# Optimization experiments

Measured on AMD Instinct MI355X. Metric: run time of the kernel, lower is better.

Reference implementation:

```python
import jax, jax.numpy as jnp
import numpy as np

BETA, ALPHA, NS_STEPS = 0.9, 1.0, 1
D_MODEL, D_STATE, D_CONV, EXPAND = 768, 16, 4, 2
D_INNER = EXPAND * D_MODEL
DT_RANK = -(-D_MODEL // 16)  # ceil(d_model/16) = 48
B, L = 2, 1024


def setup_inputs() -> dict:
    key = jax.random.key(0)
    ks = jax.random.split(key, 8)
    s = lambda k, shape, sc=0.02: jax.random.normal(k, shape, jnp.float32) * sc
    return {
        "hidden_states": jax.random.normal(ks[0], (B, L, D_MODEL), jnp.float32),
        "in_proj_w": s(ks[1], (2 * D_INNER, D_MODEL)),
        "conv_w": s(ks[2], (D_INNER, 1, D_CONV), 0.2),
        "conv_b": jnp.zeros((D_INNER,), jnp.float32),
        "x_proj_w": s(ks[3], (DT_RANK + 2 * D_STATE, D_INNER)),
        "dt_head_w": s(ks[4], (D_INNER, DT_RANK)),
        "dt_head_b": s(ks[5], (D_INNER,), 0.1),
        "out_proj_w": s(ks[6], (D_MODEL, D_INNER)),
        "D": jnp.ones((D_INNER,), jnp.float32),
    }


def _newton_schulz(G, steps):
    """Muon-style quintic Newton-Schulz orthogonalization of (b, d, n) with d >= n."""
    a, b, c = 3.4445, -4.7750, 2.0315
    X = G / (jnp.linalg.norm(G, axis=(-2, -1), keepdims=True) + 1e-7)
    X = X.swapaxes(-2, -1)  # (b, n, d): rows <= cols
    for _ in range(steps):
        A = X @ X.swapaxes(-2, -1)       # (b, n, n) small Gram
        Bm = b * A + c * (A @ A)
        X = a * X + Bm @ X
    return X.swapaxes(-2, -1)            # back to (b, d, n)


def reference(hidden_states, in_proj_w, conv_w, conv_b, x_proj_w, dt_head_w, dt_head_b, out_proj_w, D):
    Bz, Lz, _ = hidden_states.shape
    dtype = hidden_states.dtype
    # input projection -> x, z  (B, L, d_inner) each
    xz = jnp.einsum('bld,ed->ble', hidden_states, in_proj_w)
    x, z = jnp.split(xz, 2, axis=-1)
    # causal depthwise conv over time + SiLU
    xc = jax.lax.conv_general_dilated(
        x.swapaxes(1, 2), conv_w, (1,), [(D_CONV - 1, 0)],
        dimension_numbers=('NCH', 'OIH', 'NCH'), feature_group_count=D_INNER)
    x = jax.nn.silu(xc.swapaxes(1, 2) + conv_b)  # (B, L, d_inner)
    # projections for dt / k / q
    x_dbl = jnp.einsum('bld,ed->ble', x, x_proj_w)
    dt_low, k, q = jnp.split(x_dbl, [DT_RANK, DT_RANK + D_STATE], axis=-1)
    dt = jnp.einsum('blr,dr->bld', dt_low, dt_head_w)  # (B, L, d_inner), bias applied in scan

    def step(carry, inp):
        v, h = carry  # velocity / hidden states, each (b, d_inner, d_state)
        x_t, dt_t, k_t, q_t = inp
        dt_t = jax.nn.sigmoid(dt_t + dt_head_b)                              # (b, d)
        dt_t = dt_t / (1.0 + dt_t * jnp.sum(k_t * k_t, axis=-1, keepdims=True))
        dA = 1.0 - dt_t[:, :, None] * (k_t * k_t)[:, None, :]                # (b, d, n)
        G = (dt_t * x_t)[:, :, None] * k_t[:, None, :]                       # dt * u * k
        v = BETA * v + ALPHA * _newton_schulz(G, NS_STEPS)
        h = dA * h + v
        y_t = jnp.einsum('bdn,bn->bd', h, q_t) + D * x_t
        return (v, h), y_t

    init = (jnp.zeros((Bz, D_INNER, D_STATE), dtype),
            jnp.zeros((Bz, D_INNER, D_STATE), dtype))
    xs = (x.swapaxes(0, 1), dt.swapaxes(0, 1), k.swapaxes(0, 1), q.swapaxes(0, 1))
    _, y = jax.lax.scan(step, init, xs)        # (L, B, d_inner)
    y = y.swapaxes(0, 1) * jax.nn.silu(z)      # gate
    return jnp.einsum('bld,od->blo', y, out_proj_w)
```

## Files before the change

### kernel.cpp

```cpp
#include <hip/hip_runtime.h>

#define D_MODEL 768
#define D_STATE 16
#define D_INNER 1536
#define DT_RANK 48
#define NB 2
#define LSEQ 1024
#define NROWS (NB * LSEQ)
#define CCH 16
#define CLEN (LSEQ / CCH)
#define STP 16
#define BETA_CL 1.1790185e-03f
#define OUT_ELEMS (NROWS * D_MODEL)

typedef __attribute__((ext_vector_type(4))) float f32x4;
typedef __attribute__((ext_vector_type(8))) short s16x8;
typedef __attribute__((ext_vector_type(8))) unsigned short u16x8;
typedef __attribute__((ext_vector_type(4))) unsigned short u16x4;

__device__ __forceinline__ unsigned short f2bu(float f) {
  unsigned int x = __builtin_bit_cast(unsigned int, f);
  x += 0x7fffu + ((x >> 16) & 1u);
  return (unsigned short)(x >> 16);
}

typedef __attribute__((address_space(3))) unsigned int as3u32;
typedef __attribute__((address_space(1))) const unsigned int as1u32;
__device__ __forceinline__ void gload16(const unsigned short* g, unsigned short* l) {
  __builtin_amdgcn_global_load_lds((as1u32*)g, (as3u32*)l, 16, 0, 0);
}

#define CVT_TOTAL 663552
#define Z1_GROUPS 20480
__global__ __launch_bounds__(256) void cvt5z_kernel(const float* __restrict__ s0,
                                                    const float* __restrict__ s1,
                                                    const float* __restrict__ s2,
                                                    const float* __restrict__ s3,
                                                    const float* __restrict__ s4,
                                                    unsigned short* __restrict__ d0,
                                                    unsigned short* __restrict__ d1,
                                                    unsigned short* __restrict__ d2,
                                                    unsigned short* __restrict__ d3,
                                                    unsigned short* __restrict__ d4,
                                                    float* __restrict__ z1) {
  int g = blockIdx.x * 256 + threadIdx.x;
  if (g >= CVT_TOTAL) {
    int zg = g - CVT_TOTAL;
    f32x4 zero = {0.f, 0.f, 0.f, 0.f};
    if (zg < Z1_GROUPS) {
      *(f32x4*)(z1 + zg * 8) = zero;
      *(f32x4*)(z1 + zg * 8 + 4) = zero;
    }
    return;
  }
  const float* s;
  unsigned short* d;
  int base;
  if (g < 196608)      { s = s0; d = d0; base = 0; }
  else if (g < 491520) { s = s1; d = d1; base = 196608; }
  else if (g < 506880) { s = s2; d = d2; base = 491520; }
  else if (g < 516096) { s = s3; d = d3; base = 506880; }
  else                 { s = s4; d = d4; base = 516096; }
  int i = (g - base) * 8;
  f32x4 a = *(const f32x4*)(s + i);
  f32x4 b = *(const f32x4*)(s + i + 4);
  u16x8 o;
#pragma unroll
  for (int j = 0; j < 4; j++) { o[j] = f2bu(a[j]); o[4 + j] = f2bu(b[j]); }
  *(u16x8*)(d + i) = o;
}

template <bool PARTIAL>
__global__ __launch_bounds__(256) void gemm128(const unsigned short* __restrict__ A,
                                               const unsigned short* __restrict__ B,
                                               float* __restrict__ C, int K,
                                               int lda, int ldb, int ldc, int kseg_len) {
  __shared__ __align__(16) unsigned short As[2][128 * 32];
  __shared__ __align__(16) unsigned short Bs[2][128 * 32];
  const int m0 = blockIdx.y * 128, n0 = blockIdx.x * 128;
  const int kbeg = blockIdx.z * kseg_len;
  const int kend = kbeg + kseg_len;
  const int t = threadIdx.x;
  const int wave = t >> 6, lane = t & 63;
  const int wm = wave >> 1, wn = wave & 1;
  const int quad = lane >> 4, l16 = lane & 15;
  const int srow = lane >> 2;
  const int kcol = (lane & 3) * 8;

  float* Cp = C;
  if constexpr (PARTIAL) Cp = C + (size_t)blockIdx.z * (size_t)gridDim.y * 128 * ldc;

  auto stage = [&](int bi, int k0) {
#pragma unroll
    for (int r = 0; r < 2; r++) {
      const int seg = r * 64 + wave * 16;
      gload16(A + (size_t)(m0 + seg + srow) * lda + k0 + kcol, &As[bi][seg * 32]);
      gload16(B + (size_t)(n0 + seg + srow) * ldb + k0 + kcol, &Bs[bi][seg * 32]);
    }
  };

  f32x4 acc[4][4] = {};
  stage(0, kbeg);
  __syncthreads();
  int buf = 0;
  for (int k0 = kbeg; k0 < kend; k0 += 32) {
    if (k0 + 32 < kend) stage(buf ^ 1, k0 + 32);
    s16x8 af[4], bf[4];
#pragma unroll
    for (int i = 0; i < 4; i++) {
      af[i] = *(const s16x8*)&As[buf][(wm * 64 + i * 16 + l16) * 32 + quad * 8];
      bf[i] = *(const s16x8*)&Bs[buf][(wn * 64 + i * 16 + l16) * 32 + quad * 8];
    }
#pragma unroll
    for (int mi = 0; mi < 4; mi++)
#pragma unroll
      for (int ni = 0; ni < 4; ni++)
        acc[mi][ni] = __builtin_amdgcn_mfma_f32_16x16x32_bf16(af[mi], bf[ni], acc[mi][ni], 0, 0, 0);
    __syncthreads();
    buf ^= 1;
  }
#pragma unroll
  for (int mi = 0; mi < 4; mi++)
#pragma unroll
    for (int ni = 0; ni < 4; ni++)
#pragma unroll
      for (int r = 0; r < 4; r++) {
        int row = m0 + wm * 64 + mi * 16 + quad * 4 + r;
        int col = n0 + wn * 64 + ni * 16 + l16;
        Cp[(size_t)row * ldc + col] = acc[mi][ni][r];
      }
}

__global__ __launch_bounds__(256) void reduce4_kernel(const float* __restrict__ part,
                                                      float* __restrict__ out) {
  int i4 = (blockIdx.x * 256 + threadIdx.x) * 4;
  f32x4 a = *(const f32x4*)(part + i4);
  f32x4 b = *(const f32x4*)(part + (size_t)OUT_ELEMS + i4);
  f32x4 c = *(const f32x4*)(part + (size_t)2 * OUT_ELEMS + i4);
  f32x4 d = *(const f32x4*)(part + (size_t)3 * OUT_ELEMS + i4);
  f32x4 o;
#pragma unroll
  for (int j = 0; j < 4; j++) o[j] = (a[j] + b[j]) + (c[j] + d[j]);
  *(f32x4*)(out + i4) = o;
}

template <bool AF32, bool ATOMIC>
__global__ __launch_bounds__(256) void gemm_bt(const void* __restrict__ Av,
                                               const unsigned short* __restrict__ B,
                                               float* __restrict__ C, int M, int N, int K,
                                               int lda, int ldb, int ldc, int kseg_len) {
  __shared__ __align__(16) unsigned short As[2][64][40];
  __shared__ __align__(16) unsigned short Bs[2][64][40];
  const int m0 = blockIdx.y * 64, n0 = blockIdx.x * 64;
  const int kbeg = blockIdx.z * kseg_len;
  const int kend = (kbeg + kseg_len < K) ? (kbeg + kseg_len) : K;
  const int t = threadIdx.x;
  const int wave = t >> 6, lane = t & 63;
  const int wm = wave >> 1, wn = wave & 1;
  const int quad = lane >> 4, l16 = lane & 15;
  const int srow = t >> 2;
  const int kseg = (t & 3) * 8;
  const bool va = (m0 + srow) < M, vb = (n0 + srow) < N;
  const float* Af = (const float*)Av;
  const unsigned short* Ab = (const unsigned short*)Av;
  const unsigned short* Bp = B + (size_t)(n0 + srow) * ldb;

  f32x4 ra0, ra1;
  u16x8 rab, rbb;
  auto pref = [&](int k0) {
    const int kk = k0 + kseg;
    const int krem = kend - kk;
    if constexpr (AF32) {
      const float* Ap = Af + (size_t)(m0 + srow) * lda + kk;
      if (va && krem >= 8) {
        ra0 = *(const f32x4*)Ap;
        ra1 = *(const f32x4*)(Ap + 4);
      } else {
#pragma unroll
        for (int j = 0; j < 4; j++) {
          ra0[j] = (va && j < krem) ? Ap[j] : 0.0f;
          ra1[j] = (va && j + 4 < krem) ? Ap[j + 4] : 0.0f;
        }
      }
    } else {
      const unsigned short* Ap = Ab + (size_t)(m0 + srow) * lda + kk;
      if (va && krem >= 8) {
        rab = *(const u16x8*)Ap;
      } else {
#pragma unroll
        for (int j = 0; j < 8; j++) rab[j] = (va && j < krem) ? Ap[j] : (unsigned short)0;
      }
    }
    if (vb && krem >= 8) {
      rbb = *(const u16x8*)(Bp + kk);
    } else {
#pragma unroll
      for (int j = 0; j < 8; j++) rbb[j] = (vb && j < krem) ? Bp[kk + j] : (unsigned short)0;
    }
  };
  auto tolds = [&](int bi) {
    if constexpr (AF32) {
      u16x8 oa;
#pragma unroll
      for (int j = 0; j < 4; j++) { oa[j] = f2bu(ra0[j]); oa[4 + j] = f2bu(ra1[j]); }
      *(u16x8*)&As[bi][srow][kseg] = oa;
    } else {
      *(u16x8*)&As[bi][srow][kseg] = rab;
    }
    *(u16x8*)&Bs[bi][srow][kseg] = rbb;
  };

  f32x4 acc[2][2] = {};
  pref(kbeg);
  tolds(0);
  __syncthreads();
  int buf = 0;
  for (int k0 = kbeg; k0 < kend; k0 += 32) {
    const bool more = (k0 + 32 < kend);
    if (more) pref(k0 + 32);
    s16x8 a0 = *(const s16x8*)&As[buf][wm * 32 + l16][quad * 8];
    s16x8 a1 = *(const s16x8*)&As[buf][wm * 32 + 16 + l16][quad * 8];
    s16x8 b0 = *(const s16x8*)&Bs[buf][wn * 32 + l16][quad * 8];
    s16x8 b1 = *(const s16x8*)&Bs[buf][wn * 32 + 16 + l16][quad * 8];
    acc[0][0] = __builtin_amdgcn_mfma_f32_16x16x32_bf16(a0, b0, acc[0][0], 0, 0, 0);
    acc[0][1] = __builtin_amdgcn_mfma_f32_16x16x32_bf16(a0, b1, acc[0][1], 0, 0, 0);
    acc[1][0] = __builtin_amdgcn_mfma_f32_16x16x32_bf16(a1, b0, acc[1][0], 0, 0, 0);
    acc[1][1] = __builtin_amdgcn_mfma_f32_16x16x32_bf16(a1, b1, acc[1][1], 0, 0, 0);
    if (more) tolds(buf ^ 1);
    __syncthreads();
    buf ^= 1;
  }
#pragma unroll
  for (int mi = 0; mi < 2; mi++)
#pragma unroll
    for (int ni = 0; ni < 2; ni++)
#pragma unroll
      for (int r = 0; r < 4; r++) {
        int row = m0 + wm * 32 + mi * 16 + quad * 4 + r;
        int col = n0 + wn * 32 + ni * 16 + l16;
        if (row < M && col < N) {
          if constexpr (ATOMIC)
            atomicAdd(&C[(size_t)row * ldc + col], acc[mi][ni][r]);
          else
            C[(size_t)row * ldc + col] = acc[mi][ni][r];
        }
      }
}

__global__ __launch_bounds__(256) void conv_silu_kernel(const float* __restrict__ xz,
                                                        const float* __restrict__ cw,
                                                        const float* __restrict__ cb,
                                                        float* __restrict__ xc,
                                                        unsigned short* __restrict__ xcb) {
  int g = blockIdx.x * 256 + threadIdx.x;
  int c4 = (g % 384) * 4;
  int row = g / 384;
  int l = row & (LSEQ - 1);
  f32x4 acc = *(const f32x4*)(cb + c4);
  f32x4 w[4];
#pragma unroll
  for (int ci = 0; ci < 4; ci++) w[ci] = *(const f32x4*)(cw + (c4 + ci) * 4);
#pragma unroll
  for (int j = 0; j < 4; j++) {
    int dl = l - 3 + j;
    if (dl >= 0) {
      f32x4 xv = *(const f32x4*)(xz + (size_t)(row - 3 + j) * 3072 + c4);
#pragma unroll
      for (int ci = 0; ci < 4; ci++) acc[ci] = fmaf(xv[ci], w[ci][j], acc[ci]);
    }
  }
  f32x4 val;
  u16x4 ob;
#pragma unroll
  for (int ci = 0; ci < 4; ci++) {
    float sg = 1.0f / (1.0f + expf(-acc[ci]));
    val[ci] = acc[ci] * sg;
    ob[ci] = f2bu(val[ci]);
  }
  *(f32x4*)(xc + (size_t)row * D_INNER + c4) = val;
  *(u16x4*)(xcb + (size_t)row * D_INNER + c4) = ob;
}

__global__ __launch_bounds__(256) void precompute_kernel(const float* __restrict__ xdbl,
                                                         float* __restrict__ dtbuf,
                                                         const float* __restrict__ xconv,
                                                         const float* __restrict__ dtb,
                                                         float* __restrict__ ubuf,
                                                         float* __restrict__ kqbuf) {
  int row = blockIdx.x;
  int t = threadIdx.x;
  const float* xr = xdbl + (size_t)row * 80;
  float nk = 0.0f;
#pragma unroll
  for (int n = 0; n < 16; n++) { float kv = xr[48 + n]; nk += kv * kv; }
  f32x4 dtf[2], u0[2];
  float nupart = 0.0f;
#pragma unroll
  for (int gi = 0; gi < 2; gi++) {
    int g = gi * 256 + t;
    if (g < 384) {
      int d = g * 4;
      f32x4 draw = *(const f32x4*)(dtbuf + (size_t)row * D_INNER + d);
      f32x4 bb = *(const f32x4*)(dtb + d);
      f32x4 xcv = *(const f32x4*)(xconv + (size_t)row * D_INNER + d);
      f32x4 df, uu;
#pragma unroll
      for (int j = 0; j < 4; j++) {
        float sg = 1.0f / (1.0f + expf(-(draw[j] + bb[j])));
        float dv = sg / (1.0f + sg * nk);
        df[j] = dv;
        float u = dv * xcv[j];
        uu[j] = u;
        nupart += u * u;
      }
      dtf[gi] = df;
      u0[gi] = uu;
    }
  }
  __shared__ float red[4];
  float v = nupart;
#pragma unroll
  for (int off = 32; off > 0; off >>= 1) v += __shfl_xor(v, off);
  if ((t & 63) == 0) red[t >> 6] = v;
  __syncthreads();
  float nu = red[0] + red[1] + red[2] + red[3];
  float p = nu * nk;
  float s = sqrtf(p) + 1e-7f;
  float tt = p / (s * s);
  float gamma = (3.4445f + tt * (-4.7750f + 2.0315f * tt)) / s;
#pragma unroll
  for (int gi = 0; gi < 2; gi++) {
    int g = gi * 256 + t;
    if (g < 384) {
      int d = g * 4;
      f32x4 df = dtf[gi], uu = u0[gi], us;
#pragma unroll
      for (int j = 0; j < 4; j++) us[j] = gamma * uu[j];
      *(f32x4*)(dtbuf + (size_t)row * D_INNER + d) = df;
      *(f32x4*)(ubuf + (size_t)row * D_INNER + d) = us;
    }
  }
  if (t < 8)
    *(f32x4*)(kqbuf + (size_t)row * 32 + t * 4) = *(const f32x4*)(xr + 48 + t * 4);
}

__global__ __launch_bounds__(256) void scan_phase1(const float* __restrict__ ubuf,
                                                   const float* __restrict__ dtbuf,
                                                   const float* __restrict__ kqbuf,
                                                   float* __restrict__ cvp,
                                                   float* __restrict__ chp,
                                                   float* __restrict__ gp,
                                                   float* __restrict__ rp) {
  __shared__ __align__(16) float u_s[2][STP][64];
  __shared__ __align__(16) float dt_s[2][STP][64];
  __shared__ __align__(16) float kq_s[2][STP][36];
  const int t = threadIdx.x;
  const int nq = t & 3, dloc = t >> 2;
  const int b = blockIdx.x / (24 * CCH);
  const int rem = blockIdx.x % (24 * CCH);
  const int d0 = (rem / CCH) * 64;
  const int c = rem % CCH;
  const int tbase = c * CLEN;
  const size_t ub = (size_t)b * LSEQ * D_INNER + d0;
  const float* kqb = kqbuf + (size_t)b * LSEQ * 32;
  const int prow = t >> 4, pcol = (t & 15) * 4;
  const int krow = t >> 3, kcol = (t & 7) * 4;
  f32x4 pu, pd, pk;
  auto prefetch = [&](int t0) {
    size_t off = ub + (size_t)(t0 + prow) * D_INNER + pcol;
    pu = *(const f32x4*)(ubuf + off);
    pd = *(const f32x4*)(dtbuf + off);
    if (t < 128) pk = *(const f32x4*)(kqb + (size_t)(t0 + krow) * 32 + kcol);
  };
  auto writelds = [&](int bi) {
    *(f32x4*)&u_s[bi][prow][pcol] = pu;
    *(f32x4*)&dt_s[bi][prow][pcol] = pd;
    if (t < 128) *(f32x4*)&kq_s[bi][krow][kcol] = pk;
  };
  f32x4 v = {0.f, 0.f, 0.f, 0.f}, h = {0.f, 0.f, 0.f, 0.f};
  f32x4 g = {0.f, 0.f, 0.f, 0.f}, r = {1.f, 1.f, 1.f, 1.f};
  float bt = 0.9f;
  prefetch(tbase);
  writelds(0);
  __syncthreads();
  int buf = 0;
  for (int t0 = 0; t0 < CLEN; t0 += STP) {
    const bool more = (t0 + STP < CLEN);
    if (more) prefetch(tbase + t0 + STP);
#pragma unroll 4
    for (int s = 0; s < STP; s++) {
      float u = u_s[buf][s][dloc];
      float dtf = dt_s[buf][s][dloc];
      f32x4 kv = *(const f32x4*)&kq_s[buf][s][nq * 4];
#pragma unroll
      for (int j = 0; j < 4; j++) {
        float kj = kv[j];
        v[j] = fmaf(0.9f, v[j], u * kj);
        float a = fmaf(-dtf * kj, kj, 1.0f);
        h[j] = fmaf(a, h[j], v[j]);
        r[j] *= a;
        g[j] = fmaf(a, g[j], bt);
      }
      bt *= 0.9f;
    }
    if (more) writelds(buf ^ 1);
    __syncthreads();
    buf ^= 1;
  }
  size_t o = (((size_t)b * CCH + c) * D_INNER + d0 + dloc) * 16 + nq * 4;
  *(f32x4*)(cvp + o) = v;
  *(f32x4*)(chp + o) = h;
  *(f32x4*)(gp + o) = g;
  *(f32x4*)(rp + o) = r;
}

__global__ __launch_bounds__(256) void scan_phase2(const float* __restrict__ cvp,
                                                   const float* __restrict__ chp,
                                                   float* __restrict__ gp,
                                                   float* __restrict__ rp) {
  int i4 = (blockIdx.x * 256 + threadIdx.x) * 4;
  int b = i4 / (D_INNER * 16);
  int rem = i4 % (D_INNER * 16);
  f32x4 v0 = {0.f, 0.f, 0.f, 0.f}, h0 = {0.f, 0.f, 0.f, 0.f};
#pragma unroll
  for (int c = 0; c < CCH; c++) {
    size_t o = ((size_t)(b * CCH + c)) * (D_INNER * 16) + rem;
    f32x4 cv = *(const f32x4*)(cvp + o);
    f32x4 ch = *(const f32x4*)(chp + o);
    f32x4 gg = *(const f32x4*)(gp + o);
    f32x4 rr = *(const f32x4*)(rp + o);
    *(f32x4*)(gp + o) = v0;
    *(f32x4*)(rp + o) = h0;
#pragma unroll
    for (int j = 0; j < 4; j++) {
      float v0n = fmaf(BETA_CL, v0[j], cv[j]);
      float h0n = fmaf(gg[j], v0[j], fmaf(rr[j], h0[j], ch[j]));
      v0[j] = v0n;
      h0[j] = h0n;
    }
  }
}

__global__ __launch_bounds__(256) void scan_phase3(const float* __restrict__ ubuf,
                                                   const float* __restrict__ dtbuf,
                                                   const float* __restrict__ kqbuf,
                                                   const float* __restrict__ gp,
                                                   const float* __restrict__ rp,
                                                   const float* __restrict__ xconv,
                                                   const float* __restrict__ xz,
                                                   const float* __restrict__ Dp,
                                                   unsigned short* __restrict__ ygb) {
  __shared__ __align__(16) float u_s[2][STP][64];
  __shared__ __align__(16) float dt_s[2][STP][64];
  __shared__ __align__(16) float xc_s[2][STP][64];
  __shared__ __align__(16) float z_s[2][STP][64];
  __shared__ __align__(16) float kq_s[2][STP][36];
  const int t = threadIdx.x;
  const int nq = t & 3, dloc = t >> 2;
  const int b = blockIdx.x / (24 * CCH);
  const int rem = blockIdx.x % (24 * CCH);
  const int d0 = (rem / CCH) * 64;
  const int c = rem % CCH;
  const int tbase = c * CLEN;
  const size_t ub = (size_t)b * LSEQ * D_INNER + d0;
  const float* kqb = kqbuf + (size_t)b * LSEQ * 32;
  const float* xzb = xz + (size_t)b * LSEQ * 3072 + 1536 + d0;
  unsigned short* y_p = ygb + (size_t)b * LSEQ * D_INNER + d0 + dloc;
  const int prow = t >> 4, pcol = (t & 15) * 4;
  const int krow = t >> 3, kcol = (t & 7) * 4;
  f32x4 pu, pd, pxc, pz, pk;
  auto prefetch = [&](int t0) {
    size_t off = ub + (size_t)(t0 + prow) * D_INNER + pcol;
    pu = *(const f32x4*)(ubuf + off);
    pd = *(const f32x4*)(dtbuf + off);
    pxc = *(const f32x4*)(xconv + off);
    pz = *(const f32x4*)(xzb + (size_t)(t0 + prow) * 3072 + pcol);
    if (t < 128) pk = *(const f32x4*)(kqb + (size_t)(t0 + krow) * 32 + kcol);
  };
  auto writelds = [&](int bi) {
    *(f32x4*)&u_s[bi][prow][pcol] = pu;
    *(f32x4*)&dt_s[bi][prow][pcol] = pd;
    *(f32x4*)&xc_s[bi][prow][pcol] = pxc;
    *(f32x4*)&z_s[bi][prow][pcol] = pz;
    if (t < 128) *(f32x4*)&kq_s[bi][krow][kcol] = pk;
  };
  size_t so = (((size_t)b * CCH + c) * D_INNER + d0 + dloc) * 16 + nq * 4;
  f32x4 v = *(const f32x4*)(gp + so);
  f32x4 h = *(const f32x4*)(rp + so);
  const float Dd = Dp[d0 + dloc];
  prefetch(tbase);
  writelds(0);
  __syncthreads();
  int buf = 0;
  for (int t0 = 0; t0 < CLEN; t0 += STP) {
    const bool more = (t0 + STP < CLEN);
    if (more) prefetch(tbase + t0 + STP);
#pragma unroll 4
    for (int s = 0; s < STP; s++) {
      float u = u_s[buf][s][dloc];
      float dtf = dt_s[buf][s][dloc];
      f32x4 kv = *(const f32x4*)&kq_s[buf][s][nq * 4];
      f32x4 qv = *(const f32x4*)&kq_s[buf][s][16 + nq * 4];
      float yp = 0.0f;
#pragma unroll
      for (int j = 0; j < 4; j++) {
        float kj = kv[j];
        v[j] = fmaf(0.9f, v[j], u * kj);
        float dA = fmaf(-dtf * kj, kj, 1.0f);
        h[j] = fmaf(dA, h[j], v[j]);
        yp = fmaf(h[j], qv[j], yp);
      }
      yp += __shfl_xor(yp, 1);
      yp += __shfl_xor(yp, 2);
      float zv = z_s[buf][s][dloc];
      float sz = zv / (1.0f + expf(-zv));
      float val = (yp + Dd * xc_s[buf][s][dloc]) * sz;
      if (nq == 0) y_p[(size_t)(tbase + t0 + s) * D_INNER] = f2bu(val);
    }
    if (more) writelds(buf ^ 1);
    __syncthreads();
    buf ^= 1;
  }
}

extern "C" void kernel_launch(void* const* d_in, const int* in_sizes, int n_in,
                              void* d_out, int out_size, void* d_ws, size_t ws_size,
                              hipStream_t stream) {
  const float* hidden = (const float*)d_in[0];
  const float* w_in   = (const float*)d_in[1];
  const float* conv_w = (const float*)d_in[2];
  const float* conv_b = (const float*)d_in[3];
  const float* w_x    = (const float*)d_in[4];
  const float* w_dt   = (const float*)d_in[5];
  const float* b_dt   = (const float*)d_in[6];
  const float* w_out  = (const float*)d_in[7];
  const float* Dp     = (const float*)d_in[8];

  float* ws    = (float*)d_ws;
  float* xz    = ws;
  float* xconv = xz + (size_t)NROWS * 3072;
  float* xdbl  = xconv + (size_t)NROWS * D_INNER;
  float* dtbuf = xdbl + (size_t)NROWS * 80;
  float* ubuf  = dtbuf + (size_t)NROWS * D_INNER;
  float* kqbuf = ubuf + (size_t)NROWS * D_INNER;
  const size_t PL = (size_t)NB * CCH * D_INNER * 16;
  float* cvp   = kqbuf + (size_t)NROWS * 32;
  float* chp   = cvp + PL;
  float* gp    = chp + PL;
  float* rp    = gp + PL;
  float* opart = rp + PL;
  unsigned short* bfr = (unsigned short*)(opart + (size_t)4 * OUT_ELEMS);
  unsigned short* hbf = bfr;
  unsigned short* wib = hbf + 1572864;
  unsigned short* wxb = wib + 2359296;
  unsigned short* wdb = wxb + 122880;
  unsigned short* wob = wdb + 73728;
  unsigned short* xcb = wob + 1179648;
  unsigned short* ygb = xcb + 3145728;

  dim3 blk(256);
  cvt5z_kernel<<<dim3((CVT_TOTAL + Z1_GROUPS) / 256), blk, 0, stream>>>(
      hidden, w_in, w_x, w_dt, w_out, hbf, wib, wxb, wdb, wob, xdbl);
  gemm128<false><<<dim3(24, 16, 1), blk, 0, stream>>>(hbf, wib, xz, 768, 768, 768, 3072, 768);
  conv_silu_kernel<<<dim3(3072), blk, 0, stream>>>(xz, conv_w, conv_b, xconv, xcb);
  gemm_bt<false, true><<<dim3(2, 32, 8), blk, 0, stream>>>(xcb, wxb, xdbl, 2048, 80, 1536,
                                                           1536, 1536, 80, 192);
  gemm_bt<true, false><<<dim3(24, 32, 1), blk, 0, stream>>>(xdbl, wdb, dtbuf, 2048, 1536, 48,
                                                            80, 48, 1536, 48);
  precompute_kernel<<<dim3(NROWS), blk, 0, stream>>>(xdbl, dtbuf, xconv, b_dt, ubuf, kqbuf);
  scan_phase1<<<dim3(NB * 24 * CCH), blk, 0, stream>>>(ubuf, dtbuf, kqbuf, cvp, chp, gp, rp);
  scan_phase2<<<dim3(48), blk, 0, stream>>>(cvp, chp, gp, rp);
  scan_phase3<<<dim3(NB * 24 * CCH), blk, 0, stream>>>(ubuf, dtbuf, kqbuf, gp, rp,
                                                       xconv, xz, Dp, ygb);
  gemm128<true><<<dim3(6, 16, 4), blk, 0, stream>>>(ygb, wob, opart, 1536,
                                                    1536, 1536, 768, 384);
  reduce4_kernel<<<dim3(OUT_ELEMS / 1024), blk, 0, stream>>>(opart, (float*)d_out);
}
```

Baseline: 203.4 us.

## Split-K the input projection and recompute scaled u inside the scan

The input-projection GEMM becomes a two-way split-K into two partial buffers. The conv and the phase-3 z loads now sum the two partials on the fly instead of a separate reduce. The precompute kernel no longer writes a full gamma-scaled u tensor; it stores one gamma per row. Both scan phases rebuild u as gamma*dt*xconv from data they already stage in shared memory. This removes one full-size intermediate write and read and adds parallelism to the GEMM, at the cost of doubling the reads of the xz partials.

```diff
diff --git a/kernel.cpp b/kernel.cpp
--- a/kernel.cpp
+++ b/kernel.cpp
@@ -247,7 +247,7 @@
       }
 }
 
-__global__ __launch_bounds__(256) void conv_silu_kernel(const float* __restrict__ xz,
+__global__ __launch_bounds__(256) void conv_silu_kernel(const float* __restrict__ xzp,
                                                         const float* __restrict__ cw,
                                                         const float* __restrict__ cb,
                                                         float* __restrict__ xc,
@@ -256,6 +256,8 @@
   int c4 = (g % 384) * 4;
   int row = g / 384;
   int l = row & (LSEQ - 1);
+  const float* x0 = xzp;
+  const float* x1 = xzp + (size_t)NROWS * 3072;
   f32x4 acc = *(const f32x4*)(cb + c4);
   f32x4 w[4];
 #pragma unroll
@@ -264,9 +266,11 @@
   for (int j = 0; j < 4; j++) {
     int dl = l - 3 + j;
     if (dl >= 0) {
-      f32x4 xv = *(const f32x4*)(xz + (size_t)(row - 3 + j) * 3072 + c4);
-#pragma unroll
-      for (int ci = 0; ci < 4; ci++) acc[ci] = fmaf(xv[ci], w[ci][j], acc[ci]);
+      size_t off = (size_t)(row - 3 + j) * 3072 + c4;
+      f32x4 a0 = *(const f32x4*)(x0 + off);
+      f32x4 a1 = *(const f32x4*)(x1 + off);
+#pragma unroll
+      for (int ci = 0; ci < 4; ci++) acc[ci] = fmaf(a0[ci] + a1[ci], w[ci][j], acc[ci]);
     }
   }
   f32x4 val;
@@ -285,7 +289,7 @@
                                                          float* __restrict__ dtbuf,
                                                          const float* __restrict__ xconv,
                                                          const float* __restrict__ dtb,
-                                                         float* __restrict__ ubuf,
+                                                         float* __restrict__ gammabuf,
                                                          float* __restrict__ kqbuf) {
   int row = blockIdx.x;
   int t = threadIdx.x;
@@ -293,7 +297,6 @@
   float nk = 0.0f;
 #pragma unroll
   for (int n = 0; n < 16; n++) { float kv = xr[48 + n]; nk += kv * kv; }
-  f32x4 dtf[2], u0[2];
   float nupart = 0.0f;
 #pragma unroll
   for (int gi = 0; gi < 2; gi++) {
@@ -303,18 +306,16 @@
       f32x4 draw = *(const f32x4*)(dtbuf + (size_t)row * D_INNER + d);
       f32x4 bb = *(const f32x4*)(dtb + d);
       f32x4 xcv = *(const f32x4*)(xconv + (size_t)row * D_INNER + d);
-      f32x4 df, uu;
+      f32x4 df;
 #pragma unroll
       for (int j = 0; j < 4; j++) {
         float sg = 1.0f / (1.0f + expf(-(draw[j] + bb[j])));
         float dv = sg / (1.0f + sg * nk);
         df[j] = dv;
         float u = dv * xcv[j];
-        uu[j] = u;
         nupart += u * u;
       }
-      dtf[gi] = df;
-      u0[gi] = uu;
+      *(f32x4*)(dtbuf + (size_t)row * D_INNER + d) = df;
     }
   }
   __shared__ float red[4];
@@ -328,32 +329,23 @@
   float s = sqrtf(p) + 1e-7f;
   float tt = p / (s * s);
   float gamma = (3.4445f + tt * (-4.7750f + 2.0315f * tt)) / s;
-#pragma unroll
-  for (int gi = 0; gi < 2; gi++) {
-    int g = gi * 256 + t;
-    if (g < 384) {
-      int d = g * 4;
-      f32x4 df = dtf[gi], uu = u0[gi], us;
-#pragma unroll
-      for (int j = 0; j < 4; j++) us[j] = gamma * uu[j];
-      *(f32x4*)(dtbuf + (size_t)row * D_INNER + d) = df;
-      *(f32x4*)(ubuf + (size_t)row * D_INNER + d) = us;
-    }
-  }
+  if (t == 0) gammabuf[row] = gamma;
   if (t < 8)
     *(f32x4*)(kqbuf + (size_t)row * 32 + t * 4) = *(const f32x4*)(xr + 48 + t * 4);
 }
 
-__global__ __launch_bounds__(256) void scan_phase1(const float* __restrict__ ubuf,
+__global__ __launch_bounds__(256) void scan_phase1(const float* __restrict__ xconv,
                                                    const float* __restrict__ dtbuf,
                                                    const float* __restrict__ kqbuf,
+                                                   const float* __restrict__ gammabuf,
                                                    float* __restrict__ cvp,
                                                    float* __restrict__ chp,
                                                    float* __restrict__ gp,
                                                    float* __restrict__ rp) {
-  __shared__ __align__(16) float u_s[2][STP][64];
+  __shared__ __align__(16) float xc_s[2][STP][64];
   __shared__ __align__(16) float dt_s[2][STP][64];
   __shared__ __align__(16) float kq_s[2][STP][36];
+  __shared__ float g_s[2][STP];
   const int t = threadIdx.x;
   const int nq = t & 3, dloc = t >> 2;
   const int b = blockIdx.x / (24 * CCH);
@@ -361,40 +353,43 @@
   const int d0 = (rem / CCH) * 64;
   const int c = rem % CCH;
   const int tbase = c * CLEN;
-  const size_t ub = (size_t)b * LSEQ * D_INNER + d0;
-  const float* kqb = kqbuf + (size_t)b * LSEQ * 32;
+  const size_t ub = ((size_t)b * LSEQ + tbase) * D_INNER + d0;
+  const float* kqb = kqbuf + ((size_t)b * LSEQ + tbase) * 32;
+  const float* gmb = gammabuf + (size_t)b * LSEQ + tbase;
   const int prow = t >> 4, pcol = (t & 15) * 4;
   const int krow = t >> 3, kcol = (t & 7) * 4;
-  f32x4 pu, pd, pk;
+  f32x4 pxc, pd, pk;
+  float pg;
   auto prefetch = [&](int t0) {
     size_t off = ub + (size_t)(t0 + prow) * D_INNER + pcol;
-    pu = *(const f32x4*)(ubuf + off);
+    pxc = *(const f32x4*)(xconv + off);
     pd = *(const f32x4*)(dtbuf + off);
     if (t < 128) pk = *(const f32x4*)(kqb + (size_t)(t0 + krow) * 32 + kcol);
+    if (t < STP) pg = gmb[t0 + t];
   };
   auto writelds = [&](int bi) {
-    *(f32x4*)&u_s[bi][prow][pcol] = pu;
+    *(f32x4*)&xc_s[bi][prow][pcol] = pxc;
     *(f32x4*)&dt_s[bi][prow][pcol] = pd;
     if (t < 128) *(f32x4*)&kq_s[bi][krow][kcol] = pk;
+    if (t < STP) g_s[bi][t] = pg;
   };
   f32x4 v = {0.f, 0.f, 0.f, 0.f}, h = {0.f, 0.f, 0.f, 0.f};
   f32x4 g = {0.f, 0.f, 0.f, 0.f}, r = {1.f, 1.f, 1.f, 1.f};
   float bt = 0.9f;
-  prefetch(tbase);
+  prefetch(0);
   writelds(0);
   __syncthreads();
   int buf = 0;
   for (int t0 = 0; t0 < CLEN; t0 += STP) {
     const bool more = (t0 + STP < CLEN);
-    if (more) prefetch(tbase + t0 + STP);
+    if (more) prefetch(t0 + STP);
 #pragma unroll 4
     for (int s = 0; s < STP; s++) {
-      float u = u_s[buf][s][dloc];
       float dtf = dt_s[buf][s][dloc];
-      f32x4 kv = *(const f32x4*)&kq_s[buf][s][nq * 4];
+      float u = g_s[buf][s] * dtf * xc_s[buf][s][dloc];
 #pragma unroll
       for (int j = 0; j < 4; j++) {
-        float kj = kv[j];
+        float kj = kq_s[buf][s][nq * 4 + j];
         v[j] = fmaf(0.9f, v[j], u * kj);
         float a = fmaf(-dtf * kj, kj, 1.0f);
         h[j] = fmaf(a, h[j], v[j]);
@@ -441,20 +436,20 @@
   }
 }
 
-__global__ __launch_bounds__(256) void scan_phase3(const float* __restrict__ ubuf,
-                                                   const float* __restrict__ dtbuf,
+__global__ __launch_bounds__(256) void scan_phase3(const float* __restrict__ dtbuf,
                                                    const float* __restrict__ kqbuf,
+                                                   const float* __restrict__ gammabuf,
                                                    const float* __restrict__ gp,
                                                    const float* __restrict__ rp,
                                                    const float* __restrict__ xconv,
-                                                   const float* __restrict__ xz,
+                                                   const float* __restrict__ xzp,
                                                    const float* __restrict__ Dp,
                                                    unsigned short* __restrict__ ygb) {
-  __shared__ __align__(16) float u_s[2][STP][64];
+  __shared__ __align__(16) float xc_s[2][STP][64];
   __shared__ __align__(16) float dt_s[2][STP][64];
-  __shared__ __align__(16) float xc_s[2][STP][64];
   __shared__ __align__(16) float z_s[2][STP][64];
   __shared__ __align__(16) float kq_s[2][STP][36];
+  __shared__ float g_s[2][STP];
   const int t = threadIdx.x;
   const int nq = t & 3, dloc = t >> 2;
   const int b = blockIdx.x / (24 * CCH);
@@ -462,43 +457,51 @@
   const int d0 = (rem / CCH) * 64;
   const int c = rem % CCH;
   const int tbase = c * CLEN;
-  const size_t ub = (size_t)b * LSEQ * D_INNER + d0;
-  const float* kqb = kqbuf + (size_t)b * LSEQ * 32;
-  const float* xzb = xz + (size_t)b * LSEQ * 3072 + 1536 + d0;
+  const size_t ub = ((size_t)b * LSEQ + tbase) * D_INNER + d0;
+  const float* kqb = kqbuf + ((size_t)b * LSEQ + tbase) * 32;
+  const float* gmb = gammabuf + (size_t)b * LSEQ + tbase;
+  const float* z0 = xzp + ((size_t)b * LSEQ + tbase) * 3072 + 1536 + d0;
+  const float* z1 = z0 + (size_t)NROWS * 3072;
   unsigned short* y_p = ygb + (size_t)b * LSEQ * D_INNER + d0 + dloc;
   const int prow = t >> 4, pcol = (t & 15) * 4;
   const int krow = t >> 3, kcol = (t & 7) * 4;
-  f32x4 pu, pd, pxc, pz, pk;
+  f32x4 pxc, pd, pz, pk;
+  float pg;
   auto prefetch = [&](int t0) {
     size_t off = ub + (size_t)(t0 + prow) * D_INNER + pcol;
-    pu = *(const f32x4*)(ubuf + off);
+    pxc = *(const f32x4*)(xconv + off);
     pd = *(const f32x4*)(dtbuf + off);
-    pxc = *(const f32x4*)(xconv + off);
-    pz = *(const f32x4*)(xzb + (size_t)(t0 + prow) * 3072 + pcol);
+    size_t zoff = (size_t)(t0 + prow) * 3072 + pcol;
+    f32x4 a0 = *(const f32x4*)(z0 + zoff);
+    f32x4 a1 = *(const f32x4*)(z1 + zoff);
+#pragma unroll
+    for (int j = 0; j < 4; j++) pz[j] = a0[j] + a1[j];
     if (t < 128) pk = *(const f32x4*)(kqb + (size_t)(t0 + krow) * 32 + kcol);
+    if (t < STP) pg = gmb[t0 + t];
   };
   auto writelds = [&](int bi) {
-    *(f32x4*)&u_s[bi][prow][pcol] = pu;
+    *(f32x4*)&xc_s[bi][prow][pcol] = pxc;
     *(f32x4*)&dt_s[bi][prow][pcol] = pd;
-    *(f32x4*)&xc_s[bi][prow][pcol] = pxc;
     *(f32x4*)&z_s[bi][prow][pcol] = pz;
     if (t < 128) *(f32x4*)&kq_s[bi][krow][kcol] = pk;
+    if (t < STP) g_s[bi][t] = pg;
   };
   size_t so = (((size_t)b * CCH + c) * D_INNER + d0 + dloc) * 16 + nq * 4;
   f32x4 v = *(const f32x4*)(gp + so);
   f32x4 h = *(const f32x4*)(rp + so);
   const float Dd = Dp[d0 + dloc];
-  prefetch(tbase);
+  prefetch(0);
   writelds(0);
   __syncthreads();
   int buf = 0;
   for (int t0 = 0; t0 < CLEN; t0 += STP) {
     const bool more = (t0 + STP < CLEN);
-    if (more) prefetch(tbase + t0 + STP);
+    if (more) prefetch(t0 + STP);
 #pragma unroll 4
     for (int s = 0; s < STP; s++) {
-      float u = u_s[buf][s][dloc];
+      float xcv = xc_s[buf][s][dloc];
       float dtf = dt_s[buf][s][dloc];
+      float u = g_s[buf][s] * dtf * xcv;
       f32x4 kv = *(const f32x4*)&kq_s[buf][s][nq * 4];
       f32x4 qv = *(const f32x4*)&kq_s[buf][s][16 + nq * 4];
       float yp = 0.0f;
@@ -514,7 +517,7 @@
       yp += __shfl_xor(yp, 2);
       float zv = z_s[buf][s][dloc];
       float sz = zv / (1.0f + expf(-zv));
-      float val = (yp + Dd * xc_s[buf][s][dloc]) * sz;
+      float val = (yp + Dd * xcv) * sz;
       if (nq == 0) y_p[(size_t)(tbase + t0 + s) * D_INNER] = f2bu(val);
     }
     if (more) writelds(buf ^ 1);
@@ -537,12 +540,12 @@
   const float* Dp     = (const float*)d_in[8];
 
   float* ws    = (float*)d_ws;
-  float* xz    = ws;
-  float* xconv = xz + (size_t)NROWS * 3072;
+  float* xzp   = ws;
+  float* xconv = xzp + (size_t)2 * NROWS * 3072;
   float* xdbl  = xconv + (size_t)NROWS * D_INNER;
   float* dtbuf = xdbl + (size_t)NROWS * 80;
-  float* ubuf  = dtbuf + (size_t)NROWS * D_INNER;
-  float* kqbuf = ubuf + (size_t)NROWS * D_INNER;
+  float* gammabuf = dtbuf + (size_t)NROWS * D_INNER;
+  float* kqbuf = gammabuf + NROWS;
   const size_t PL = (size_t)NB * CCH * D_INNER * 16;
   float* cvp   = kqbuf + (size_t)NROWS * 32;
   float* chp   = cvp + PL;
@@ -561,17 +564,18 @@
   dim3 blk(256);
   cvt5z_kernel<<<dim3((CVT_TOTAL + Z1_GROUPS) / 256), blk, 0, stream>>>(
       hidden, w_in, w_x, w_dt, w_out, hbf, wib, wxb, wdb, wob, xdbl);
-  gemm128<false><<<dim3(24, 16, 1), blk, 0, stream>>>(hbf, wib, xz, 768, 768, 768, 3072, 768);
-  conv_silu_kernel<<<dim3(3072), blk, 0, stream>>>(xz, conv_w, conv_b, xconv, xcb);
+  gemm128<true><<<dim3(24, 16, 2), blk, 0, stream>>>(hbf, wib, xzp, 768, 768, 768, 3072, 384);
+  conv_silu_kernel<<<dim3(3072), blk, 0, stream>>>(xzp, conv_w, conv_b, xconv, xcb);
   gemm_bt<false, true><<<dim3(2, 32, 8), blk, 0, stream>>>(xcb, wxb, xdbl, 2048, 80, 1536,
                                                            1536, 1536, 80, 192);
   gemm_bt<true, false><<<dim3(24, 32, 1), blk, 0, stream>>>(xdbl, wdb, dtbuf, 2048, 1536, 48,
                                                             80, 48, 1536, 48);
-  precompute_kernel<<<dim3(NROWS), blk, 0, stream>>>(xdbl, dtbuf, xconv, b_dt, ubuf, kqbuf);
-  scan_phase1<<<dim3(NB * 24 * CCH), blk, 0, stream>>>(ubuf, dtbuf, kqbuf, cvp, chp, gp, rp);
+  precompute_kernel<<<dim3(NROWS), blk, 0, stream>>>(xdbl, dtbuf, xconv, b_dt, gammabuf, kqbuf);
+  scan_phase1<<<dim3(NB * 24 * CCH), blk, 0, stream>>>(xconv, dtbuf, kqbuf, gammabuf,
+                                                       cvp, chp, gp, rp);
   scan_phase2<<<dim3(48), blk, 0, stream>>>(cvp, chp, gp, rp);
-  scan_phase3<<<dim3(NB * 24 * CCH), blk, 0, stream>>>(ubuf, dtbuf, kqbuf, gp, rp,
-                                                       xconv, xz, Dp, ygb);
+  scan_phase3<<<dim3(NB * 24 * CCH), blk, 0, stream>>>(dtbuf, kqbuf, gammabuf, gp, rp,
+                                                       xconv, xzp, Dp, ygb);
   gemm128<true><<<dim3(6, 16, 4), blk, 0, stream>>>(ygb, wob, opart, 1536,
                                                     1536, 1536, 768, 384);
   reduce4_kernel<<<dim3(OUT_ELEMS / 1024), blk, 0, stream>>>(opart, (float*)d_out);
```

New measurement: 212.8 us. 1.05x slower.
